# Optimization experiments

Measured on AMD Instinct MI355X. Metric: run time of the kernel, lower is better.

Reference implementation:

```python
import jax, jax.numpy as jnp
import numpy as np

B_, H_, N_, L_ = 4, 512, 64, 2048  # batch, d_model, d_state/2 (conj pairs), seq len


def setup_inputs() -> dict:
    key = jax.random.key(0)
    ks = jax.random.split(key, 8)
    x = jax.random.normal(ks[0], (B_, H_, L_), jnp.float32)
    ln_w = jnp.ones((H_,), jnp.float32)
    ln_b = jnp.zeros((H_,), jnp.float32)
    # S4D-style init: dt log-uniform in [1e-3, 1e-1], A = -1/2 + i*pi*n (S4D-Lin)
    log_dt = jax.random.uniform(ks[1], (H_,), jnp.float32) * (np.log(0.1) - np.log(0.001)) + np.log(0.001)
    log_A_real = jnp.broadcast_to(jnp.log(jnp.float32(0.5)), (H_, N_))
    A_imag = jnp.broadcast_to(np.pi * jnp.arange(N_, dtype=np.float32), (H_, N_))
    B_re = jnp.ones((H_, N_), jnp.float32)
    B_im = jnp.zeros((H_, N_), jnp.float32)
    # 2 kernel channels for bidirectional
    C_re = jax.random.normal(ks[2], (2, H_, N_), jnp.float32) * (0.5 ** 0.5)
    C_im = jax.random.normal(ks[3], (2, H_, N_), jnp.float32) * (0.5 ** 0.5)
    D = jax.random.normal(ks[4], (H_,), jnp.float32)
    W_out = jax.random.normal(ks[5], (H_, H_), jnp.float32) / np.sqrt(H_)
    b_out = jnp.zeros((H_,), jnp.float32)
    return dict(x=x, ln_w=ln_w, ln_b=ln_b, log_dt=log_dt, log_A_real=log_A_real,
                A_imag=A_imag, B_re=B_re, B_im=B_im, C_re=C_re, C_im=C_im,
                D=D, W_out=W_out, b_out=b_out)


def _s4_layer(x, ln_w, ln_b, log_dt, log_A_real, A_imag, B_re, B_im, C_re, C_im, D, W_out, b_out):
    Bb, H, L = x.shape
    # ---- pre-norm LayerNorm over channel dim (module transposes to (B,L,H)) ----
    zt = x.transpose(0, 2, 1)                          # (B, L, H)
    mu = zt.mean(-1, keepdims=True)
    var = jnp.mean((zt - mu) ** 2, -1, keepdims=True)
    zt = (zt - mu) * jax.lax.rsqrt(var + 1e-5) * ln_w + ln_b
    z = zt.transpose(0, 2, 1)                          # (B, H, L)
    # ---- S4 diagonal SSM kernel, ZOH discretization, 2 channels (bidirectional) ----
    dt = jnp.exp(log_dt)[:, None]                      # (H, 1)
    A = -jnp.exp(log_A_real) + 1j * A_imag             # (H, N)
    dtA = A * dt                                       # (H, N)
    dB = (B_re + 1j * B_im) * (jnp.exp(dtA) - 1.0) / A # (H, N) discretized B
    CB = (C_re + 1j * C_im) * dB                       # (2, H, N)
    V = jnp.exp(dtA[:, :, None] * jnp.arange(L))       # (H, N, L) Vandermonde exp(l*dt*A)
    k = 2.0 * jnp.real(jnp.einsum('chn,hnl->chl', CB, V))  # (2, H, L)
    # ---- bidirectional: causal + flipped anticausal kernel, length 2L ----
    zpad = jnp.zeros_like(k[0])
    kb = jnp.concatenate([k[0], zpad], -1) + jnp.concatenate([zpad, k[1][:, ::-1]], -1)  # (H, 2L)
    # ---- FFT convolution ----
    k_f = jnp.fft.rfft(kb, n=2 * L)                    # (H, L+1)
    u_f = jnp.fft.rfft(z, n=2 * L)                     # (B, H, L+1)
    y = jnp.fft.irfft(u_f * k_f, n=2 * L)[..., :L]     # (B, H, L)
    y = y + z * D[:, None]                             # skip connection D*u
    y = jax.nn.gelu(y)                                 # default S4 activation
    y = jnp.einsum('oh,bhl->bol', W_out, y) + b_out[:, None]  # output linear (Conv1d k=1)
    return y + x                                       # residual of S4Layer


def reference(x, ln_w, ln_b, log_dt, log_A_real, A_imag, B_re, B_im, C_re, C_im, D, W_out, b_out):
    return _s4_layer(x, ln_w, ln_b, log_dt, log_A_real, A_imag, B_re, B_im, C_re, C_im, D, W_out, b_out)
```

## Files before the change

### kernel.cpp

```cpp
#include <hip/hip_runtime.h>
#include <math.h>

#define Bq 4
#define Hq 512
#define Nq 64
#define Lq 2048
#define PARAM (Hq*Nq)

__global__ void prep_kernel(const float* __restrict__ log_dt,
                            const float* __restrict__ log_A_real,
                            const float* __restrict__ A_imag,
                            const float* __restrict__ B_re, const float* __restrict__ B_im,
                            const float* __restrict__ C_re, const float* __restrict__ C_im,
                            float* __restrict__ wr_, float* __restrict__ wi_,
                            float* __restrict__ a0, float* __restrict__ b0,
                            float* __restrict__ a1, float* __restrict__ b1) {
    int idx = blockIdx.x * blockDim.x + threadIdx.x;
    if (idx >= PARAM) return;
    int h = idx >> 6;
    float dt = expf(log_dt[h]);
    float Ar = -expf(log_A_real[idx]);
    float Ai = A_imag[idx];
    float er = expf(Ar * dt);
    float wr = er * cosf(Ai * dt);
    float wi = er * sinf(Ai * dt);
    wr_[idx] = wr; wi_[idx] = wi;
    float mr = wr - 1.0f, mi = wi;
    float den = Ar * Ar + Ai * Ai;
    float qr = (mr * Ar + mi * Ai) / den;
    float qi = (mi * Ar - mr * Ai) / den;
    float Br = B_re[idx], Bi = B_im[idx];
    float dBr = Br * qr - Bi * qi;
    float dBi = Br * qi + Bi * qr;
    float cr = C_re[idx], ci = C_im[idx];
    a0[idx] =  2.0f * (cr * dBr - ci * dBi);
    b0[idx] = -2.0f * (cr * dBi + ci * dBr);
    cr = C_re[PARAM + idx]; ci = C_im[PARAM + idx];
    a1[idx] =  2.0f * (cr * dBr - ci * dBi);
    b1[idx] = -2.0f * (cr * dBi + ci * dBr);
}

__global__ __launch_bounds__(256)
void ln_kernel(const float* __restrict__ x, const float* __restrict__ lnw,
               const float* __restrict__ lnb, float* __restrict__ z) {
    int blk = blockIdx.x;
    int b  = blk / (Lq / 16);
    int l0 = (blk % (Lq / 16)) * 16;
    int tx = threadIdx.x & 15;
    int ty = threadIdx.x >> 4;
    const float* xb = x + (size_t)b * Hq * Lq;
    float s = 0.f, s2 = 0.f;
    for (int h = ty; h < Hq; h += 16) {
        float v = xb[h * Lq + l0 + tx];
        s += v; s2 += v * v;
    }
    __shared__ float rs_[16][17], r2_[16][17], mu_s[16], sg_s[16];
    rs_[ty][tx] = s; r2_[ty][tx] = s2;
    __syncthreads();
    if (ty == 0) {
        float a = 0.f, c = 0.f;
        #pragma unroll
        for (int i = 0; i < 16; ++i) { a += rs_[i][tx]; c += r2_[i][tx]; }
        float mu = a * (1.0f / Hq);
        float var = c * (1.0f / Hq) - mu * mu;
        mu_s[tx] = mu;
        sg_s[tx] = rsqrtf(var + 1e-5f);
    }
    __syncthreads();
    float mu = mu_s[tx], rs = sg_s[tx];
    float* zb = z + (size_t)b * Hq * Lq;
    for (int h = ty; h < Hq; h += 16) {
        float v = xb[h * Lq + l0 + tx];
        zb[h * Lq + l0 + tx] = (v - mu) * rs * lnw[h] + lnb[h];
    }
}

template <int DIR>
__device__ __forceinline__ void scan_body(const float* __restrict__ zz,
                                          float* __restrict__ yout,
                                          float wr, float wi, float a, float b,
                                          float (*tile)[33], float* zbuf, int n) {
    float sr = 0.f, si = 0.f;
    for (int q0 = 0; q0 < Lq; q0 += 32) {
        if (n < 32) zbuf[n] = zz[DIR ? (Lq - 1 - q0 - n) : (q0 + n)];
        __syncthreads();
        float p[32];
        #pragma unroll
        for (int k = 0; k < 32; ++k) {
            float zt = zbuf[k];
            if (DIR == 0) {
                float t1 = fmaf(wi, si, -zt);
                float t2 = wi * sr;
                sr = fmaf(wr, sr, -t1);
                si = fmaf(wr, si, t2);
                p[k] = fmaf(a, sr, b * si);
            } else {
                p[k] = fmaf(a, sr, b * si);
                float t1 = fmaf(wi, si, -zt);
                float t2 = wi * sr;
                sr = fmaf(wr, sr, -t1);
                si = fmaf(wr, si, t2);
            }
        }
        #pragma unroll
        for (int k = 0; k < 32; ++k) tile[n][k] = p[k];
        __syncthreads();
        int tloc = n & 31, ih = n >> 5;
        float acc = 0.f;
        #pragma unroll
        for (int j = 0; j < 32; ++j) acc += tile[ih * 32 + j][tloc];
        acc += __shfl_xor(acc, 32, 64);
        if (n < 32) yout[DIR ? (Lq - 1 - q0 - n) : (q0 + n)] = acc;
    }
}

__global__ __launch_bounds__(64)
void scan_kernel(const float* __restrict__ z,
                 const float* __restrict__ wr_, const float* __restrict__ wi_,
                 const float* __restrict__ a0, const float* __restrict__ b0,
                 const float* __restrict__ a1, const float* __restrict__ b1,
                 float* __restrict__ y0, float* __restrict__ y1) {
    int bh  = blockIdx.x;
    int dir = blockIdx.y;
    int h = bh & (Hq - 1);
    int n = threadIdx.x;
    int pidx = h * Nq + n;
    float wr = wr_[pidx], wi = wi_[pidx];
    __shared__ float tile[64][33];
    __shared__ float zbuf[32];
    const float* zz = z + (size_t)bh * Lq;
    if (dir == 0) {
        scan_body<0>(zz, y0 + (size_t)bh * Lq, wr, wi, a0[pidx], b0[pidx], tile, zbuf, n);
    } else {
        scan_body<1>(zz, y1 + (size_t)bh * Lq, wr, wi, a1[pidx], b1[pidx], tile, zbuf, n);
    }
}

__global__ __launch_bounds__(256)
void act_kernel(float4* __restrict__ y0, const float4* __restrict__ y1,
                const float4* __restrict__ z, const float* __restrict__ D) {
    int i4 = blockIdx.x * 256 + threadIdx.x;
    int h = (i4 >> 9) & (Hq - 1);
    float d = D[h];
    float4 v0 = y0[i4], v1 = y1[i4], vz = z[i4];
    float vv[4] = { v0.x + v1.x + d * vz.x, v0.y + v1.y + d * vz.y,
                    v0.z + v1.z + d * vz.z, v0.w + v1.w + d * vz.w };
    #pragma unroll
    for (int i = 0; i < 4; ++i) {
        float v = vv[i];
        float t = tanhf(0.7978845608028654f * (v + 0.044715f * v * v * v));
        vv[i] = 0.5f * v * (1.0f + t);
    }
    float4 r; r.x = vv[0]; r.y = vv[1]; r.z = vv[2]; r.w = vv[3];
    y0[i4] = r;
}

__global__ __launch_bounds__(256)
void gemm_kernel(const float* __restrict__ u, const float* __restrict__ W,
                 const float* __restrict__ bias, const float* __restrict__ x,
                 float* __restrict__ out) {
    int l0 = blockIdx.x * 64;
    int o0 = blockIdx.y * 128;
    int b  = blockIdx.z;
    int tid = threadIdx.x;
    __shared__ float Ws[16][129];
    __shared__ float Us[16][65];
    const float* ub = u + (size_t)b * Hq * Lq;
    float acc[8][4] = {};
    int wo = tid >> 4, wl = tid & 15;
    for (int k0 = 0; k0 < Hq; k0 += 16) {
        {
            int j  = tid & 15;
            int ib = tid >> 4;
            #pragma unroll
            for (int r = 0; r < 8; ++r) {
                int i = ib + 16 * r;
                Ws[j][i] = W[(size_t)(o0 + i) * Hq + k0 + j];
            }
            int li = tid & 63;
            int jb = tid >> 6;
            #pragma unroll
            for (int r = 0; r < 4; ++r) {
                int j2 = jb + 4 * r;
                Us[j2][li] = ub[(size_t)(k0 + j2) * Lq + l0 + li];
            }
        }
        __syncthreads();
        #pragma unroll
        for (int j = 0; j < 16; ++j) {
            float av[8], bv[4];
            #pragma unroll
            for (int i = 0; i < 8; ++i) av[i] = Ws[j][8 * wo + i];
            #pragma unroll
            for (int i = 0; i < 4; ++i) bv[i] = Us[j][4 * wl + i];
            #pragma unroll
            for (int io = 0; io < 8; ++io)
                #pragma unroll
                for (int il = 0; il < 4; ++il)
                    acc[io][il] = fmaf(av[io], bv[il], acc[io][il]);
        }
        __syncthreads();
    }
    #pragma unroll
    for (int io = 0; io < 8; ++io) {
        int o = o0 + 8 * wo + io;
        float bo = bias[o];
        size_t base = ((size_t)b * Hq + o) * Lq + l0 + 4 * wl;
        const float4 xr = *(const float4*)(x + base);
        float4 r;
        r.x = acc[io][0] + bo + xr.x;
        r.y = acc[io][1] + bo + xr.y;
        r.z = acc[io][2] + bo + xr.z;
        r.w = acc[io][3] + bo + xr.w;
        *(float4*)(out + base) = r;
    }
}

extern "C" void kernel_launch(void* const* d_in, const int* in_sizes, int n_in,
                              void* d_out, int out_size, void* d_ws, size_t ws_size,
                              hipStream_t stream) {
    (void)in_sizes; (void)n_in; (void)out_size; (void)ws_size;
    const float* x          = (const float*)d_in[0];
    const float* ln_w       = (const float*)d_in[1];
    const float* ln_b       = (const float*)d_in[2];
    const float* log_dt     = (const float*)d_in[3];
    const float* log_A_real = (const float*)d_in[4];
    const float* A_imag     = (const float*)d_in[5];
    const float* B_re       = (const float*)d_in[6];
    const float* B_im       = (const float*)d_in[7];
    const float* C_re       = (const float*)d_in[8];
    const float* C_im       = (const float*)d_in[9];
    const float* Dv         = (const float*)d_in[10];
    const float* W          = (const float*)d_in[11];
    const float* b_out      = (const float*)d_in[12];
    float* out = (float*)d_out;
    float* ws  = (float*)d_ws;

    float* wr = ws;
    float* wi = ws + PARAM;
    float* a0 = ws + 2 * PARAM;
    float* b0 = ws + 3 * PARAM;
    float* a1 = ws + 4 * PARAM;
    float* b1 = ws + 5 * PARAM;
    float* z  = ws + 6 * PARAM;
    float* y0 = z  + (size_t)Bq * Hq * Lq;
    float* y1 = y0 + (size_t)Bq * Hq * Lq;

    prep_kernel<<<PARAM / 256, 256, 0, stream>>>(log_dt, log_A_real, A_imag,
                                                 B_re, B_im, C_re, C_im,
                                                 wr, wi, a0, b0, a1, b1);
    ln_kernel<<<Bq * (Lq / 16), 256, 0, stream>>>(x, ln_w, ln_b, z);
    scan_kernel<<<dim3(Bq * Hq, 2), 64, 0, stream>>>(z, wr, wi, a0, b0, a1, b1, y0, y1);
    act_kernel<<<(Bq * Hq * Lq / 4) / 256, 256, 0, stream>>>((float4*)y0, (const float4*)y1,
                                                             (const float4*)z, Dv);
    gemm_kernel<<<dim3(Lq / 64, Hq / 128, Bq), 256, 0, stream>>>(y0, W, b_out, x, out);
}
```

Before: 322.0 us.

## Fuse bidirectional scans into one block with packed math, fold GELU in

The scan kernel now runs the forward and backward recurrences in the same block, holding both directions in two-wide float vectors so packed FMAs can be used, and it stages both z streams in one shared buffer. The separate activation kernel is removed: each scan block applies the D skip term and a fast exp-based tanh GELU to its own row, which saves one launch and a full pass over three large arrays. The backward output is stored shifted by one position to match the anticausal kernel's alignment, adding indexing complexity. The LayerNorm kernel is also retiled to 64 columns by 4 row groups for wider coalesced access. Grid parallelism for the scan is halved, so fewer blocks are available to hide latency.

```diff
diff --git a/kernel.cpp b/kernel.cpp
--- a/kernel.cpp
+++ b/kernel.cpp
@@ -6,6 +6,8 @@
 #define Nq 64
 #define Lq 2048
 #define PARAM (Hq*Nq)
+
+typedef float v2f __attribute__((ext_vector_type(2)));
 
 __global__ void prep_kernel(const float* __restrict__ log_dt,
                             const float* __restrict__ log_A_real,
@@ -43,24 +45,22 @@
 __global__ __launch_bounds__(256)
 void ln_kernel(const float* __restrict__ x, const float* __restrict__ lnw,
                const float* __restrict__ lnb, float* __restrict__ z) {
-    int blk = blockIdx.x;
-    int b  = blk / (Lq / 16);
-    int l0 = (blk % (Lq / 16)) * 16;
-    int tx = threadIdx.x & 15;
-    int ty = threadIdx.x >> 4;
+    int b  = blockIdx.x >> 5;
+    int l0 = (blockIdx.x & 31) * 64;
+    int tx = threadIdx.x & 63;
+    int ty = threadIdx.x >> 6;
     const float* xb = x + (size_t)b * Hq * Lq;
     float s = 0.f, s2 = 0.f;
-    for (int h = ty; h < Hq; h += 16) {
+    for (int h = ty; h < Hq; h += 4) {
         float v = xb[h * Lq + l0 + tx];
         s += v; s2 += v * v;
     }
-    __shared__ float rs_[16][17], r2_[16][17], mu_s[16], sg_s[16];
+    __shared__ float rs_[4][64], r2_[4][64], mu_s[64], sg_s[64];
     rs_[ty][tx] = s; r2_[ty][tx] = s2;
     __syncthreads();
     if (ty == 0) {
-        float a = 0.f, c = 0.f;
-        #pragma unroll
-        for (int i = 0; i < 16; ++i) { a += rs_[i][tx]; c += r2_[i][tx]; }
+        float a = rs_[0][tx] + rs_[1][tx] + rs_[2][tx] + rs_[3][tx];
+        float c = r2_[0][tx] + r2_[1][tx] + r2_[2][tx] + r2_[3][tx];
         float mu = a * (1.0f / Hq);
         float var = c * (1.0f / Hq) - mu * mu;
         mu_s[tx] = mu;
@@ -69,48 +69,9 @@
     __syncthreads();
     float mu = mu_s[tx], rs = sg_s[tx];
     float* zb = z + (size_t)b * Hq * Lq;
-    for (int h = ty; h < Hq; h += 16) {
+    for (int h = ty; h < Hq; h += 4) {
         float v = xb[h * Lq + l0 + tx];
         zb[h * Lq + l0 + tx] = (v - mu) * rs * lnw[h] + lnb[h];
-    }
-}
-
-template <int DIR>
-__device__ __forceinline__ void scan_body(const float* __restrict__ zz,
-                                          float* __restrict__ yout,
-                                          float wr, float wi, float a, float b,
-                                          float (*tile)[33], float* zbuf, int n) {
-    float sr = 0.f, si = 0.f;
-    for (int q0 = 0; q0 < Lq; q0 += 32) {
-        if (n < 32) zbuf[n] = zz[DIR ? (Lq - 1 - q0 - n) : (q0 + n)];
-        __syncthreads();
-        float p[32];
-        #pragma unroll
-        for (int k = 0; k < 32; ++k) {
-            float zt = zbuf[k];
-            if (DIR == 0) {
-                float t1 = fmaf(wi, si, -zt);
-                float t2 = wi * sr;
-                sr = fmaf(wr, sr, -t1);
-                si = fmaf(wr, si, t2);
-                p[k] = fmaf(a, sr, b * si);
-            } else {
-                p[k] = fmaf(a, sr, b * si);
-                float t1 = fmaf(wi, si, -zt);
-                float t2 = wi * sr;
-                sr = fmaf(wr, sr, -t1);
-                si = fmaf(wr, si, t2);
-            }
-        }
-        #pragma unroll
-        for (int k = 0; k < 32; ++k) tile[n][k] = p[k];
-        __syncthreads();
-        int tloc = n & 31, ih = n >> 5;
-        float acc = 0.f;
-        #pragma unroll
-        for (int j = 0; j < 32; ++j) acc += tile[ih * 32 + j][tloc];
-        acc += __shfl_xor(acc, 32, 64);
-        if (n < 32) yout[DIR ? (Lq - 1 - q0 - n) : (q0 + n)] = acc;
     }
 }
 
@@ -119,40 +80,71 @@
                  const float* __restrict__ wr_, const float* __restrict__ wi_,
                  const float* __restrict__ a0, const float* __restrict__ b0,
                  const float* __restrict__ a1, const float* __restrict__ b1,
+                 const float* __restrict__ Dv,
                  float* __restrict__ y0, float* __restrict__ y1) {
-    int bh  = blockIdx.x;
-    int dir = blockIdx.y;
+    int bh = blockIdx.x;
     int h = bh & (Hq - 1);
     int n = threadIdx.x;
     int pidx = h * Nq + n;
     float wr = wr_[pidx], wi = wi_[pidx];
-    __shared__ float tile[64][33];
-    __shared__ float zbuf[32];
+    v2f wr2 = { wr, wr }, wi2 = { wi, wi };
+    v2f pa = { a0[pidx], a1[pidx] };
+    v2f pb = { b0[pidx], b1[pidx] };
+
+    __shared__ float tile_f[64][33];
+    __shared__ float tile_b[64][33];
+    __shared__ v2f zp[32];
+
     const float* zz = z + (size_t)bh * Lq;
-    if (dir == 0) {
-        scan_body<0>(zz, y0 + (size_t)bh * Lq, wr, wi, a0[pidx], b0[pidx], tile, zbuf, n);
-    } else {
-        scan_body<1>(zz, y1 + (size_t)bh * Lq, wr, wi, a1[pidx], b1[pidx], tile, zbuf, n);
-    }
-}
-
-__global__ __launch_bounds__(256)
-void act_kernel(float4* __restrict__ y0, const float4* __restrict__ y1,
-                const float4* __restrict__ z, const float* __restrict__ D) {
-    int i4 = blockIdx.x * 256 + threadIdx.x;
-    int h = (i4 >> 9) & (Hq - 1);
-    float d = D[h];
-    float4 v0 = y0[i4], v1 = y1[i4], vz = z[i4];
-    float vv[4] = { v0.x + v1.x + d * vz.x, v0.y + v1.y + d * vz.y,
-                    v0.z + v1.z + d * vz.z, v0.w + v1.w + d * vz.w };
-    #pragma unroll
-    for (int i = 0; i < 4; ++i) {
-        float v = vv[i];
-        float t = tanhf(0.7978845608028654f * (v + 0.044715f * v * v * v));
-        vv[i] = 0.5f * v * (1.0f + t);
-    }
-    float4 r; r.x = vv[0]; r.y = vv[1]; r.z = vv[2]; r.w = vv[3];
-    y0[i4] = r;
+    float* y0r = y0 + (size_t)bh * Lq;
+    float* y1r = y1 + (size_t)bh * Lq;
+
+    v2f sr = {0.f, 0.f}, si = {0.f, 0.f};
+    int tloc = n & 31, ih = n >> 5;
+
+    for (int q0 = 0; q0 < Lq; q0 += 32) {
+        if (n < 32) ((float*)zp)[2 * n]            = zz[q0 + n];
+        else        ((float*)zp)[2 * (n - 32) + 1] = zz[Lq - 1 - q0 - (n - 32)];
+        __syncthreads();
+        #pragma unroll
+        for (int k = 0; k < 32; ++k) {
+            v2f zt = zp[k];
+            v2f t1 = __builtin_elementwise_fma(wi2, si, -zt);
+            v2f t2 = wi2 * sr;
+            sr = __builtin_elementwise_fma(wr2, sr, -t1);
+            si = __builtin_elementwise_fma(wr2, si, t2);
+            v2f p = __builtin_elementwise_fma(pa, sr, pb * si);
+            tile_f[n][k] = p.x;
+            tile_b[n][k] = p.y;
+        }
+        __syncthreads();
+        float af = 0.f, ab = 0.f;
+        #pragma unroll
+        for (int j = 0; j < 32; ++j) {
+            af += tile_f[ih * 32 + j][tloc];
+            ab += tile_b[ih * 32 + j][tloc];
+        }
+        af += __shfl_xor(af, 32, 64);
+        ab += __shfl_xor(ab, 32, 64);
+        if (n < 32) {
+            y0r[q0 + n] = af;
+        } else {
+            int pos = Lq - 2 - q0 - (n - 32);
+            if (pos >= 0) y1r[pos] = ab;
+        }
+    }
+    __syncthreads();
+    float d = Dv[h];
+    for (int t = n; t < Lq; t += 64) {
+        float v0 = y0r[t];
+        float v1 = (t == Lq - 1) ? 0.f : y1r[t];
+        float v = v0 + v1 + d * zz[t];
+        float g = 0.7978845608028654f * (v + 0.044715f * v * v * v);
+        g = fminf(fmaxf(g, -15.f), 15.f);
+        float e = __expf(2.0f * g);
+        float th = (e - 1.0f) * __builtin_amdgcn_rcpf(e + 1.0f);
+        y0r[t] = 0.5f * v * (1.0f + th);
+    }
 }
 
 __global__ __launch_bounds__(256)
@@ -249,9 +241,7 @@
     prep_kernel<<<PARAM / 256, 256, 0, stream>>>(log_dt, log_A_real, A_imag,
                                                  B_re, B_im, C_re, C_im,
                                                  wr, wi, a0, b0, a1, b1);
-    ln_kernel<<<Bq * (Lq / 16), 256, 0, stream>>>(x, ln_w, ln_b, z);
-    scan_kernel<<<dim3(Bq * Hq, 2), 64, 0, stream>>>(z, wr, wi, a0, b0, a1, b1, y0, y1);
-    act_kernel<<<(Bq * Hq * Lq / 4) / 256, 256, 0, stream>>>((float4*)y0, (const float4*)y1,
-                                                             (const float4*)z, Dv);
+    ln_kernel<<<Bq * (Lq / 64), 256, 0, stream>>>(x, ln_w, ln_b, z);
+    scan_kernel<<<Bq * Hq, 64, 0, stream>>>(z, wr, wi, a0, b0, a1, b1, Dv, y0, y1);
     gemm_kernel<<<dim3(Lq / 64, Hq / 128, Bq), 256, 0, stream>>>(y0, W, b_out, x, out);
 }
```

Result: slower. 364.5 us (+13.2%).
